# Performance work log

Hardware: AMD Instinct MI355X
Metric: run time of the kernel (lower is better)

## Reference

```python
import jax, jax.numpy as jnp
import numpy as np
from jax import lax

TEMPERATURE = 34.0
PAD = 1

def setup_inputs() -> dict:
    key = jax.random.key(0)
    ks = jax.random.split(key, 6)
    B, C, H, W = 16, 256, 64, 64
    K, O, kk, hidden = 4, 256, 3, int(256 * 0.25) + 1
    return {
        "x": jax.random.normal(ks[0], (B, C, H, W), jnp.float32),
        "w_fc1": jax.random.normal(ks[1], (hidden, C), jnp.float32) * 0.05,
        "w_fc2": jax.random.normal(ks[2], (K, hidden), jnp.float32) * 0.05,
        "b_fc2": jax.random.normal(ks[3], (K,), jnp.float32) * 0.05,
        "weight": jax.random.normal(ks[4], (K, O, C, kk, kk), jnp.float32) * 0.05,
        "bias": jax.random.normal(ks[5], (K, O), jnp.float32) * 0.05,
    }

def reference(x, w_fc1, w_fc2, b_fc2, weight, bias):
    # attention2d: global avg pool -> 1x1 conv -> relu -> 1x1 conv -> softmax(logits/T)
    pooled = jnp.mean(x, axis=(2, 3))                       # [B, C]
    h = jax.nn.relu(pooled @ w_fc1.T)                       # [B, hidden]
    logits = h @ w_fc2.T + b_fc2                            # [B, K]
    att = jax.nn.softmax(logits / TEMPERATURE, axis=1)      # [B, K]

    K = weight.shape[0]
    # per-sample aggregated kernels/bias
    agg_w = jnp.einsum('bk,koihw->boihw', att, weight)      # [B, O, C, k, k]
    agg_b = att @ bias                                      # [B, O]

    def conv_one(xi, wi):
        # xi: [C, H, W], wi: [O, C, k, k]
        return lax.conv_general_dilated(
            xi[None], wi, window_strides=(1, 1),
            padding=[(PAD, PAD), (PAD, PAD)],
            dimension_numbers=('NCHW', 'OIHW', 'NCHW'))[0]

    out = jax.vmap(conv_one)(x, agg_w)                      # [B, O, H, W]
    return out + agg_b[:, :, None, None]
```

## Files before the change

### kernel.cpp

```cpp
#include <hip/hip_runtime.h>
#include <math.h>

constexpr int B   = 16;
constexpr int C   = 256;
constexpr int H   = 64;
constexpr int W   = 64;
constexpr int K   = 4;
constexpr int O   = 256;
constexpr int HID = 65;
constexpr float TEMP = 34.0f;

typedef __bf16 bf16x8 __attribute__((ext_vector_type(8)));
typedef float  f32x16 __attribute__((ext_vector_type(16)));
typedef unsigned short ushort_t;

__device__ inline ushort_t f2bf(float f) {
    union { float f; unsigned u; } v; v.f = f;
    unsigned u = v.u;
    u += 0x7FFF + ((u >> 16) & 1);
    return (ushort_t)(u >> 16);
}

__device__ inline void gl2lds16(const void* g, void* l) {
    __builtin_amdgcn_global_load_lds(
        (const __attribute__((address_space(1))) unsigned int*)g,
        (__attribute__((address_space(3))) unsigned int*)l, 16, 0, 0);
}

__global__ void tp_kernel(const float* __restrict__ x,
                          ushort_t* __restrict__ xT,
                          float* __restrict__ pooled) {
    const int ci = blockIdx.x, b = blockIdx.y;
    const int tid = threadIdx.x;
    const int lane = tid & 63;

    __shared__ ushort_t t2[8 * 64 * 18];
    __shared__ float pool_l[16];
    if (tid < 16) pool_l[tid] = 0.f;
    __syncthreads();

    const float* xbase = x + ((size_t)b * C + ci * 16) * (H * W);

    for (int yg = 0; yg < 8; ++yg) {
        #pragma unroll
        for (int j = 0; j < 8; ++j) {
            const int idx = j * 256 + tid;
            const int xq = idx & 15;
            const int y8 = (idx >> 4) & 7;
            const int c  = idx >> 7;
            float4 v = *(const float4*)(xbase + ((size_t)c * H + (yg * 8 + y8)) * W + xq * 4);
            float s = (v.x + v.y) + (v.z + v.w);
            s += __shfl_xor(s, 1, 64);
            s += __shfl_xor(s, 2, 64);
            s += __shfl_xor(s, 4, 64);
            s += __shfl_xor(s, 8, 64);
            if ((lane & 15) == 0) atomicAdd(&pool_l[c], s);
            ushort_t* d = &t2[(y8 * 64 + xq * 4) * 18 + c];
            d[0]  = f2bf(v.x);
            d[18] = f2bf(v.y);
            d[36] = f2bf(v.z);
            d[54] = f2bf(v.w);
        }
        __syncthreads();
        #pragma unroll
        for (int q = 0; q < 4; ++q) {
            const int e = q * 256 + tid;
            const int y8 = e >> 7, col = (e >> 1) & 63, half = e & 1;
            const ushort_t* s0 = &t2[(y8 * 64 + col) * 18 + half * 8];
            uint4 vv;
            vv.x = *(const unsigned*)(s0 + 0);
            vv.y = *(const unsigned*)(s0 + 2);
            vv.z = *(const unsigned*)(s0 + 4);
            vv.w = *(const unsigned*)(s0 + 6);
            size_t go = (((size_t)(b * 16 + ci) * 64) + (yg * 8 + y8)) * 1024
                      + col * 16 + half * 8;
            *(uint4*)(xT + go) = vv;
        }
        __syncthreads();
    }
    if (tid < 16) pooled[b * C + ci * 16 + tid] = pool_l[tid] * (1.0f / (H * W));
}

__global__ void attention_kernel(const float* __restrict__ pooled,
                                 const float* __restrict__ w_fc1,
                                 const float* __restrict__ w_fc2,
                                 const float* __restrict__ b_fc2,
                                 float* __restrict__ att) {
    const int b = blockIdx.x;
    const int tid = threadIdx.x;
    __shared__ float pool_s[C];
    __shared__ float h_s[HID];
    __shared__ float logit_s[K];

    for (int i = tid; i < C; i += blockDim.x) pool_s[i] = pooled[b * C + i];
    __syncthreads();
    for (int j = tid; j < HID; j += blockDim.x) {
        const float* wr = w_fc1 + (size_t)j * C;
        float s = 0.f;
        #pragma unroll 4
        for (int c = 0; c < C; ++c) s += pool_s[c] * wr[c];
        h_s[j] = fmaxf(s, 0.f);
    }
    __syncthreads();
    if (tid < K) {
        const float* wr = w_fc2 + (size_t)tid * HID;
        float s = b_fc2[tid];
        for (int j = 0; j < HID; ++j) s += h_s[j] * wr[j];
        logit_s[tid] = s * (1.0f / TEMP);
    }
    __syncthreads();
    if (tid == 0) {
        float m = fmaxf(fmaxf(logit_s[0], logit_s[1]), fmaxf(logit_s[2], logit_s[3]));
        float e0 = expf(logit_s[0] - m), e1 = expf(logit_s[1] - m);
        float e2 = expf(logit_s[2] - m), e3 = expf(logit_s[3] - m);
        float inv = 1.0f / (e0 + e1 + e2 + e3);
        att[b * K + 0] = e0 * inv; att[b * K + 1] = e1 * inv;
        att[b * K + 2] = e2 * inv; att[b * K + 3] = e3 * inv;
    }
}

__global__ void wagg_kernel(const float* __restrict__ weight,
                            const float* __restrict__ att,
                            ushort_t* __restrict__ wagg_sw) {
    const int o = blockIdx.x;
    const int tid = threadIdx.x;
    const int oct = tid >> 3;
    const int bg  = tid & 7;

    __shared__ float att_s[B * K];
    if (tid < B * K) att_s[tid] = att[tid];
    __syncthreads();

    const int mi   = o >> 5;
    const int lm   = o & 31;
    const int ci   = oct >> 1;
    const int half = oct & 1;
    const int lane = half * 32 + lm;

    for (int t = 0; t < 9; ++t) {
        float w0[8], w1[8], w2[8], w3[8];
        #pragma unroll
        for (int j = 0; j < 8; ++j) {
            const size_t cidx = (size_t)(oct * 8 + j) * 9 + t;
            w0[j] = weight[((size_t)(0 * O + o) * C) * 9 + cidx];
            w1[j] = weight[((size_t)(1 * O + o) * C) * 9 + cidx];
            w2[j] = weight[((size_t)(2 * O + o) * C) * 9 + cidx];
            w3[j] = weight[((size_t)(3 * O + o) * C) * 9 + cidx];
        }
        #pragma unroll
        for (int bb = 0; bb < 2; ++bb) {
            const int b = bg * 2 + bb;
            const float a0 = att_s[b * K + 0], a1 = att_s[b * K + 1];
            const float a2 = att_s[b * K + 2], a3 = att_s[b * K + 3];
            union { ushort_t u[8]; uint4 v; } pk;
            #pragma unroll
            for (int j = 0; j < 8; ++j)
                pk.u[j] = f2bf(a0 * w0[j] + a1 * w1[j] + a2 * w2[j] + a3 * w3[j]);
            size_t idx = ((((size_t)b * 16 + ci) * 9 + t) * 8 + mi) * 512 + lane * 8;
            *(uint4*)&wagg_sw[idx] = pk.v;
        }
    }
}

__global__ __launch_bounds__(256, 2)
void conv_mfma_kernel(const ushort_t* __restrict__ xT,
                      const ushort_t* __restrict__ wagg_sw,
                      const float* __restrict__ bias,
                      const float* __restrict__ att,
                      float* __restrict__ out) {
    const int b  = blockIdx.x;
    const int yt = blockIdx.y;
    const int oz = blockIdx.z;
    const int y0 = yt * 4;

    const int tid  = threadIdx.x;
    const int lane = tid & 63;
    const int wid  = tid >> 6;
    const int n16  = lane & 31;
    const int khalf = lane >> 5;

    __shared__ __align__(16) ushort_t A_lds[9 * 4 * 512];
    __shared__ __align__(16) ushort_t x_lds[6 * 1056];

    for (int i = tid; i < 6 * 1056; i += 256) x_lds[i] = 0;

    f32x16 acc[4][2];
    #pragma unroll
    for (int a = 0; a < 4; ++a)
        #pragma unroll
        for (int ni = 0; ni < 2; ++ni)
            acc[a][ni] = (f32x16)(0.f);

    for (int ci = 0; ci < 16; ++ci) {
        __syncthreads();

        for (int i = wid; i < 36; i += 4) {
            const int t = i >> 2, a = i & 3;
            const ushort_t* g = wagg_sw
                + ((((size_t)b * 16 + ci) * 9 + t) * 8 + (oz * 4 + a)) * 512 + lane * 8;
            gl2lds16(g, &A_lds[(t * 4 + a) * 512]);
        }
        for (int r = wid; r < 6; r += 4) {
            const int y = y0 - 1 + r;
            if ((unsigned)y < (unsigned)H) {
                const ushort_t* gr = xT + (((size_t)(b * 16 + ci) * 64 + y) * 1024);
                #pragma unroll
                for (int h = 0; h < 2; ++h)
                    gl2lds16(gr + lane * 16 + h * 8,
                             &x_lds[r * 1056 + h * 528 + 8]);
            }
        }

        __syncthreads();

        #pragma unroll
        for (int dy = 0; dy < 3; ++dy) {
            const int r = wid + dy;
            #pragma unroll
            for (int dx = 0; dx < 3; ++dx) {
                const int t = dy * 3 + dx;
                bf16x8 bf[2];
                #pragma unroll
                for (int ni = 0; ni < 2; ++ni)
                    bf[ni] = *(const bf16x8*)&x_lds[r * 1056 + khalf * 528
                              + (ni * 32 + n16 + dx) * 8];
                #pragma unroll
                for (int a = 0; a < 4; ++a) {
                    bf16x8 af = *(const bf16x8*)&A_lds[(t * 4 + a) * 512 + lane * 8];
                    acc[a][0] = __builtin_amdgcn_mfma_f32_32x32x16_bf16(af, bf[0], acc[a][0], 0, 0, 0);
                    acc[a][1] = __builtin_amdgcn_mfma_f32_32x32x16_bf16(af, bf[1], acc[a][1], 0, 0, 0);
                }
            }
        }
    }

    __syncthreads();
    float* aggb = (float*)A_lds;
    if (tid < 128) {
        const int o = oz * 128 + tid;
        aggb[tid] = att[b * K + 0] * bias[0 * O + o] + att[b * K + 1] * bias[1 * O + o]
                  + att[b * K + 2] * bias[2 * O + o] + att[b * K + 3] * bias[3 * O + o];
    }
    __syncthreads();

    const int y = y0 + wid;
    #pragma unroll
    for (int a = 0; a < 4; ++a) {
        #pragma unroll
        for (int ni = 0; ni < 2; ++ni) {
            #pragma unroll
            for (int reg = 0; reg < 16; ++reg) {
                const int row = (reg & 3) + 8 * (reg >> 2) + 4 * khalf;
                const int ol  = a * 32 + row;
                out[(((size_t)b * O + oz * 128 + ol) * H + y) * W + ni * 32 + n16]
                    = acc[a][ni][reg] + aggb[ol];
            }
        }
    }
}

__global__ void pool_kernel(const float* __restrict__ x, float* __restrict__ pooled) {
    const int bc = blockIdx.x;
    const float4* p4 = (const float4*)(x + (size_t)bc * (H * W));
    const int tid = threadIdx.x;
    float s = 0.f;
    #pragma unroll
    for (int i = 0; i < (H * W / 4) / 256; ++i) {
        float4 v = p4[tid + i * 256];
        s += (v.x + v.y) + (v.z + v.w);
    }
    #pragma unroll
    for (int off = 32; off > 0; off >>= 1) s += __shfl_down(s, off, 64);
    __shared__ float red[4];
    if ((tid & 63) == 0) red[tid >> 6] = s;
    __syncthreads();
    if (tid == 0) pooled[bc] = ((red[0] + red[1]) + (red[2] + red[3])) * (1.0f / (H * W));
}

constexpr int TILE_H = 32;
constexpr int TILE_W = 64;
constexpr int CCF = 4, OT = 8, PX = 8;
constexpr int XS_STRIDE = TILE_W + 3;

__global__ __launch_bounds__(256, 2)
void conv_kernel(const float* __restrict__ x, const float* __restrict__ weight,
                 const float* __restrict__ bias, const float* __restrict__ att,
                 float* __restrict__ out) {
    const int tile_y = blockIdx.x, o0 = blockIdx.y * OT, b = blockIdx.z;
    const int tid = threadIdx.x, tx = tid & 7, ty = tid >> 3, ty0 = tile_y * TILE_H;
    __shared__ __align__(16) float xs[CCF][TILE_H + 2][XS_STRIDE];
    __shared__ __align__(16) float ws_s[OT][CCF][12];
    const float a0 = att[b * K + 0], a1 = att[b * K + 1];
    const float a2 = att[b * K + 2], a3 = att[b * K + 3];
    float acc[OT][PX];
    #pragma unroll
    for (int o = 0; o < OT; ++o)
        #pragma unroll
        for (int p = 0; p < PX; ++p) acc[o][p] = 0.f;
    const float* xb = x + (size_t)b * C * H * W;
    constexpr int X_ELEMS = CCF * (TILE_H + 2) * (TILE_W + 2);
    constexpr int W_ELEMS = OT * CCF * 9;
    for (int c0 = 0; c0 < C; c0 += CCF) {
        __syncthreads();
        for (int idx = tid; idx < X_ELEMS; idx += 256) {
            int cc = idx / ((TILE_H + 2) * (TILE_W + 2));
            int rem = idx - cc * ((TILE_H + 2) * (TILE_W + 2));
            int r = rem / (TILE_W + 2), col = rem - r * (TILE_W + 2);
            int gy = ty0 - 1 + r, gx = col - 1;
            float v = 0.f;
            if ((unsigned)gy < (unsigned)H && (unsigned)gx < (unsigned)W)
                v = xb[((size_t)(c0 + cc) * H + gy) * W + gx];
            xs[cc][r][col] = v;
        }
        for (int idx = tid; idx < W_ELEMS; idx += 256) {
            int o = idx / (CCF * 9), rem = idx - o * (CCF * 9);
            int cc = rem / 9, tap = rem - cc * 9;
            size_t base = ((size_t)(o0 + o) * C + (c0 + cc)) * 9 + tap;
            ws_s[o][cc][tap] = a0 * weight[base] + a1 * weight[(size_t)1 * O * C * 9 + base]
                             + a2 * weight[(size_t)2 * O * C * 9 + base]
                             + a3 * weight[(size_t)3 * O * C * 9 + base];
        }
        __syncthreads();
        #pragma unroll
        for (int cc = 0; cc < CCF; ++cc) {
            float xv[3][10];
            #pragma unroll
            for (int dy = 0; dy < 3; ++dy)
                #pragma unroll
                for (int j = 0; j < 10; ++j) xv[dy][j] = xs[cc][ty + dy][8 * tx + j];
            #pragma unroll
            for (int o = 0; o < OT; ++o) {
                float4 w0 = *(const float4*)&ws_s[o][cc][0];
                float4 w1 = *(const float4*)&ws_s[o][cc][4];
                float w8 = ws_s[o][cc][8];
                #pragma unroll
                for (int p = 0; p < PX; ++p) {
                    float s = acc[o][p];
                    s = fmaf(xv[0][p + 0], w0.x, s); s = fmaf(xv[0][p + 1], w0.y, s);
                    s = fmaf(xv[0][p + 2], w0.z, s); s = fmaf(xv[1][p + 0], w0.w, s);
                    s = fmaf(xv[1][p + 1], w1.x, s); s = fmaf(xv[1][p + 2], w1.y, s);
                    s = fmaf(xv[2][p + 0], w1.z, s); s = fmaf(xv[2][p + 1], w1.w, s);
                    s = fmaf(xv[2][p + 2], w8, s);
                    acc[o][p] = s;
                }
            }
        }
    }
    const int oy = ty0 + ty, ox = 8 * tx;
    #pragma unroll
    for (int o = 0; o < OT; ++o) {
        float ab = a0 * bias[0 * O + o0 + o] + a1 * bias[1 * O + o0 + o]
                 + a2 * bias[2 * O + o0 + o] + a3 * bias[3 * O + o0 + o];
        float4 v0 = make_float4(acc[o][0] + ab, acc[o][1] + ab, acc[o][2] + ab, acc[o][3] + ab);
        float4 v1 = make_float4(acc[o][4] + ab, acc[o][5] + ab, acc[o][6] + ab, acc[o][7] + ab);
        float* op = out + (((size_t)b * O + (o0 + o)) * H + oy) * W + ox;
        *(float4*)(op) = v0; *(float4*)(op + 4) = v1;
    }
}

extern "C" void kernel_launch(void* const* d_in, const int* in_sizes, int n_in,
                              void* d_out, int out_size, void* d_ws, size_t ws_size,
                              hipStream_t stream) {
    const float* x      = (const float*)d_in[0];
    const float* w_fc1  = (const float*)d_in[1];
    const float* w_fc2  = (const float*)d_in[2];
    const float* b_fc2  = (const float*)d_in[3];
    const float* weight = (const float*)d_in[4];
    const float* bias   = (const float*)d_in[5];
    float* out = (float*)d_out;

    float* pooled = (float*)d_ws;
    float* att    = pooled + B * C;
    ushort_t* wagg_sw = (ushort_t*)((char*)d_ws + 32 * 1024);
    const size_t wagg_bytes = (size_t)B * 16 * 9 * 8 * 512 * 2;
    ushort_t* xT = (ushort_t*)((char*)wagg_sw + wagg_bytes);
    const size_t xT_bytes = (size_t)B * 16 * 64 * 64 * 16 * 2;
    const size_t needed = 32 * 1024 + wagg_bytes + xT_bytes;

    if (ws_size >= needed) {
        tp_kernel<<<dim3(16, 16), dim3(256), 0, stream>>>(x, xT, pooled);
        attention_kernel<<<dim3(B), dim3(128), 0, stream>>>(pooled, w_fc1, w_fc2, b_fc2, att);
        wagg_kernel<<<dim3(O), dim3(256), 0, stream>>>(weight, att, wagg_sw);
        conv_mfma_kernel<<<dim3(B, 16, 2), dim3(256), 0, stream>>>(xT, wagg_sw, bias, att, out);
    } else {
        pool_kernel<<<dim3(B * C), dim3(256), 0, stream>>>(x, pooled);
        attention_kernel<<<dim3(B), dim3(128), 0, stream>>>(pooled, w_fc1, w_fc2, b_fc2, att);
        conv_kernel<<<dim3(H / TILE_H, O / OT, B), dim3(256), 0, stream>>>(x, weight, bias, att, out);
    }
}
```

Before: 261.2 us.

## Split transpose kernel across row groups and stage weight aggregation through LDS

The transpose/pool kernel now launches one block per 8-row group instead of looping over all row groups, which raises the grid from 256 to 2048 blocks. Partial pooled sums are combined with global atomics after a memset of the pooled buffer. The weight aggregation kernel is re-tiled by (channel group, output group). Each block loads a contiguous weight slab into LDS with float4 reads, replacing strided scalar global loads. This adds an extra memset launch, and the atomic accumulation makes the pooled sums order-dependent.

New measurement: 219.7 us. 1.19x faster.

```diff
diff --git a/kernel.cpp b/kernel.cpp
--- a/kernel.cpp
+++ b/kernel.cpp
@@ -30,55 +30,54 @@
 __global__ void tp_kernel(const float* __restrict__ x,
                           ushort_t* __restrict__ xT,
                           float* __restrict__ pooled) {
-    const int ci = blockIdx.x, b = blockIdx.y;
+    const int ci = blockIdx.x, yg = blockIdx.y, b = blockIdx.z;
     const int tid = threadIdx.x;
     const int lane = tid & 63;
 
-    __shared__ ushort_t t2[8 * 64 * 18];
+    __shared__ ushort_t t2[8 * 1154];
     __shared__ float pool_l[16];
     if (tid < 16) pool_l[tid] = 0.f;
     __syncthreads();
 
     const float* xbase = x + ((size_t)b * C + ci * 16) * (H * W);
 
-    for (int yg = 0; yg < 8; ++yg) {
-        #pragma unroll
-        for (int j = 0; j < 8; ++j) {
-            const int idx = j * 256 + tid;
-            const int xq = idx & 15;
-            const int y8 = (idx >> 4) & 7;
-            const int c  = idx >> 7;
-            float4 v = *(const float4*)(xbase + ((size_t)c * H + (yg * 8 + y8)) * W + xq * 4);
-            float s = (v.x + v.y) + (v.z + v.w);
-            s += __shfl_xor(s, 1, 64);
-            s += __shfl_xor(s, 2, 64);
-            s += __shfl_xor(s, 4, 64);
-            s += __shfl_xor(s, 8, 64);
-            if ((lane & 15) == 0) atomicAdd(&pool_l[c], s);
-            ushort_t* d = &t2[(y8 * 64 + xq * 4) * 18 + c];
-            d[0]  = f2bf(v.x);
-            d[18] = f2bf(v.y);
-            d[36] = f2bf(v.z);
-            d[54] = f2bf(v.w);
-        }
-        __syncthreads();
-        #pragma unroll
-        for (int q = 0; q < 4; ++q) {
-            const int e = q * 256 + tid;
-            const int y8 = e >> 7, col = (e >> 1) & 63, half = e & 1;
-            const ushort_t* s0 = &t2[(y8 * 64 + col) * 18 + half * 8];
-            uint4 vv;
-            vv.x = *(const unsigned*)(s0 + 0);
-            vv.y = *(const unsigned*)(s0 + 2);
-            vv.z = *(const unsigned*)(s0 + 4);
-            vv.w = *(const unsigned*)(s0 + 6);
-            size_t go = (((size_t)(b * 16 + ci) * 64) + (yg * 8 + y8)) * 1024
-                      + col * 16 + half * 8;
-            *(uint4*)(xT + go) = vv;
-        }
-        __syncthreads();
-    }
-    if (tid < 16) pooled[b * C + ci * 16 + tid] = pool_l[tid] * (1.0f / (H * W));
+    #pragma unroll
+    for (int j = 0; j < 8; ++j) {
+        const int idx = j * 256 + tid;
+        const int xq = idx & 15;
+        const int y8 = (idx >> 4) & 7;
+        const int c  = idx >> 7;
+        float4 v = *(const float4*)(xbase + ((size_t)c * H + (yg * 8 + y8)) * W + xq * 4);
+        float s = (v.x + v.y) + (v.z + v.w);
+        s += __shfl_xor(s, 1, 64);
+        s += __shfl_xor(s, 2, 64);
+        s += __shfl_xor(s, 4, 64);
+        s += __shfl_xor(s, 8, 64);
+        if ((lane & 15) == 0) atomicAdd(&pool_l[c], s);
+        ushort_t* d = &t2[y8 * 1154 + (xq * 4) * 18 + c];
+        d[0]  = f2bf(v.x);
+        d[18] = f2bf(v.y);
+        d[36] = f2bf(v.z);
+        d[54] = f2bf(v.w);
+    }
+    __syncthreads();
+
+    #pragma unroll
+    for (int q = 0; q < 4; ++q) {
+        const int e = q * 256 + tid;
+        const int y8 = e >> 7, col = (e >> 1) & 63, half = e & 1;
+        const ushort_t* s0 = &t2[y8 * 1154 + col * 18 + half * 8];
+        uint4 vv;
+        vv.x = *(const unsigned*)(s0 + 0);
+        vv.y = *(const unsigned*)(s0 + 2);
+        vv.z = *(const unsigned*)(s0 + 4);
+        vv.w = *(const unsigned*)(s0 + 6);
+        size_t go = (((size_t)(b * 16 + ci) * 64) + (yg * 8 + y8)) * 1024
+                  + col * 16 + half * 8;
+        *(uint4*)(xT + go) = vv;
+    }
+    if (tid < 16)
+        atomicAdd(&pooled[b * C + ci * 16 + tid], pool_l[tid] * (1.0f / (H * W)));
 }
 
 __global__ void attention_kernel(const float* __restrict__ pooled,
@@ -122,43 +121,45 @@
 __global__ void wagg_kernel(const float* __restrict__ weight,
                             const float* __restrict__ att,
                             ushort_t* __restrict__ wagg_sw) {
-    const int o = blockIdx.x;
+    const int ci = blockIdx.x;
+    const int mi = blockIdx.y;
     const int tid = threadIdx.x;
-    const int oct = tid >> 3;
-    const int bg  = tid & 7;
-
+    const int lane = tid & 63;
+    const int wid  = tid >> 6;
+
+    __shared__ float lds_w[4 * 32 * 145];
     __shared__ float att_s[B * K];
+
     if (tid < B * K) att_s[tid] = att[tid];
-    __syncthreads();
-
-    const int mi   = o >> 5;
-    const int lm   = o & 31;
-    const int ci   = oct >> 1;
-    const int half = oct & 1;
-    const int lane = half * 32 + lm;
-
-    for (int t = 0; t < 9; ++t) {
-        float w0[8], w1[8], w2[8], w3[8];
+
+    for (int idx = tid; idx < 128 * 36; idx += 256) {
+        const int seg = idx / 36;
+        const int off = idx - seg * 36;
+        const int k = seg >> 5, o = seg & 31;
+        const float4 v = *(const float4*)(weight
+            + ((size_t)(k * O + mi * 32 + o) * C + ci * 16) * 9 + off * 4);
+        float* d = &lds_w[seg * 145 + off * 4];
+        d[0] = v.x; d[1] = v.y; d[2] = v.z; d[3] = v.w;
+    }
+    __syncthreads();
+
+    const int o_l = lane & 31;
+    const int cc0 = (lane >> 5) * 8;
+    for (int task = wid; task < B * 9; task += 4) {
+        const int b = task / 9, t = task - b * 9;
+        const float a0 = att_s[b * K + 0], a1 = att_s[b * K + 1];
+        const float a2 = att_s[b * K + 2], a3 = att_s[b * K + 3];
+        union { ushort_t u[8]; uint4 v; } pk;
         #pragma unroll
         for (int j = 0; j < 8; ++j) {
-            const size_t cidx = (size_t)(oct * 8 + j) * 9 + t;
-            w0[j] = weight[((size_t)(0 * O + o) * C) * 9 + cidx];
-            w1[j] = weight[((size_t)(1 * O + o) * C) * 9 + cidx];
-            w2[j] = weight[((size_t)(2 * O + o) * C) * 9 + cidx];
-            w3[j] = weight[((size_t)(3 * O + o) * C) * 9 + cidx];
-        }
-        #pragma unroll
-        for (int bb = 0; bb < 2; ++bb) {
-            const int b = bg * 2 + bb;
-            const float a0 = att_s[b * K + 0], a1 = att_s[b * K + 1];
-            const float a2 = att_s[b * K + 2], a3 = att_s[b * K + 3];
-            union { ushort_t u[8]; uint4 v; } pk;
-            #pragma unroll
-            for (int j = 0; j < 8; ++j)
-                pk.u[j] = f2bf(a0 * w0[j] + a1 * w1[j] + a2 * w2[j] + a3 * w3[j]);
-            size_t idx = ((((size_t)b * 16 + ci) * 9 + t) * 8 + mi) * 512 + lane * 8;
-            *(uint4*)&wagg_sw[idx] = pk.v;
-        }
+            const int m = (cc0 + j) * 9 + t;
+            pk.u[j] = f2bf(a0 * lds_w[(0 * 32 + o_l) * 145 + m]
+                         + a1 * lds_w[(1 * 32 + o_l) * 145 + m]
+                         + a2 * lds_w[(2 * 32 + o_l) * 145 + m]
+                         + a3 * lds_w[(3 * 32 + o_l) * 145 + m]);
+        }
+        size_t idx = ((((size_t)b * 16 + ci) * 9 + t) * 8 + mi) * 512 + lane * 8;
+        *(uint4*)&wagg_sw[idx] = pk.v;
     }
 }
 
@@ -378,9 +379,10 @@
     const size_t needed = 32 * 1024 + wagg_bytes + xT_bytes;
 
     if (ws_size >= needed) {
-        tp_kernel<<<dim3(16, 16), dim3(256), 0, stream>>>(x, xT, pooled);
+        hipMemsetAsync(pooled, 0, B * C * sizeof(float), stream);
+        tp_kernel<<<dim3(16, 8, 16), dim3(256), 0, stream>>>(x, xT, pooled);
         attention_kernel<<<dim3(B), dim3(128), 0, stream>>>(pooled, w_fc1, w_fc2, b_fc2, att);
-        wagg_kernel<<<dim3(O), dim3(256), 0, stream>>>(weight, att, wagg_sw);
+        wagg_kernel<<<dim3(16, 8), dim3(256), 0, stream>>>(weight, att, wagg_sw);
         conv_mfma_kernel<<<dim3(B, 16, 2), dim3(256), 0, stream>>>(xT, wagg_sw, bias, att, out);
     } else {
         pool_kernel<<<dim3(B * C), dim3(256), 0, stream>>>(x, pooled);
```
